# Kernel tuning notes

Measured on AMD Instinct MI355X. Metric: run time of the kernel, lower is better.

The kernel has to match this reference:

```python
import jax, jax.numpy as jnp
import numpy as np

EPS = 1e-5


def setup_inputs() -> dict:
    key = jax.random.key(0)
    ks = jax.random.split(key, 8)
    B, C, D, H, O, E = 256, 64, 256, 4096, 256, 4
    x = jax.random.normal(ks[0], (B, C, D), dtype=jnp.float32)
    mask_ids = jax.random.randint(ks[1], (B, C), 0, 16)
    projection_idx = jax.random.randint(ks[2], (C,), 0, E)
    W1 = jax.random.normal(ks[3], (E, D, H), dtype=jnp.float32) * 0.02
    b1 = jnp.zeros((E, H), dtype=jnp.float32)
    gamma = jnp.ones((E, H), dtype=jnp.float32)
    beta = jnp.zeros((E, H), dtype=jnp.float32)
    W2 = jax.random.normal(ks[4], (E, H, O), dtype=jnp.float32) * 0.02
    b2 = jnp.zeros((E, O), dtype=jnp.float32)
    return {"x": x, "mask_ids": mask_ids, "projection_idx": projection_idx,
            "W1": W1, "b1": b1, "gamma": gamma, "beta": beta, "W2": W2, "b2": b2}


def reference(x, mask_ids, projection_idx, W1, b1, gamma, beta, W2, b2):
    # x: [B, C, D]; projection_idx: [C] routes each channel to one of E experts.
    # Disjoint masks => the original zeros + masked '+=' is a partition-assign.
    B, C, D = x.shape
    E, _, H = W1.shape
    # Per-channel expert params (gather once, shared over batch).
    h = jnp.einsum('bcd,cdh->bch', x, W1[projection_idx]) + b1[projection_idx]
    # BatchNorm1d in training mode: batch stats over the tokens of each expert
    # (the original flattens the selected [B, |mask|] tokens for BN).
    seg = jnp.broadcast_to(projection_idx[None, :], (B, C)).reshape(-1)  # [B*C]
    hf = h.reshape(B * C, H)
    cnt = jax.ops.segment_sum(jnp.ones((B * C,), h.dtype), seg, num_segments=E)
    cnt = jnp.maximum(cnt, 1.0)
    s1 = jax.ops.segment_sum(hf, seg, num_segments=E)            # [E, H]
    s2 = jax.ops.segment_sum(hf * hf, seg, num_segments=E)       # [E, H]
    mean = s1 / cnt[:, None]
    var = s2 / cnt[:, None] - mean * mean                        # biased var (train-mode BN)
    inv = jax.lax.rsqrt(var + EPS)
    hn = (h - mean[projection_idx]) * (inv[projection_idx] * gamma[projection_idx]) + beta[projection_idx]
    a = jax.nn.relu(hn)
    out = jnp.einsum('bch,cho->bco', a, W2[projection_idx]) + b2[projection_idx]
    return out, mask_ids
```

## Files before the change

kernel.cpp:

```cpp
#include <hip/hip_runtime.h>

typedef unsigned short u16;
typedef unsigned int   u32;
typedef __attribute__((ext_vector_type(8))) short s16x8;
typedef __attribute__((ext_vector_type(4))) float f32x4;
typedef __attribute__((ext_vector_type(4))) u32   u32x4;

#define DEV static __device__ __forceinline__

static constexpr int B_ = 256, C_ = 64, D_ = 256, H_ = 4096, O_ = 256, E_ = 4;

DEV u16 f2bf(float f) {
  u32 u = __builtin_bit_cast(u32, f);
  u += 0x7fffu + ((u >> 16) & 1u);
  return (u16)(u >> 16);
}
DEV float bf2f(u16 u) { return __builtin_bit_cast(float, (u32)u << 16); }

DEV void async16(const u16* g, u16* l) {
  __builtin_amdgcn_global_load_lds(
      (const __attribute__((address_space(1))) void*)g,
      (__attribute__((address_space(3))) void*)l, 16, 0, 0);
}

DEV int xcd_swz(int bid, int nwg) { return (bid & 7) * (nwg >> 3) + (bid >> 3); }

__global__ void k_prep(const float* __restrict__ x, u16* __restrict__ xb,
                       const float* __restrict__ W1, u16* __restrict__ w1t,
                       const float* __restrict__ W2, u16* __restrict__ w2t,
                       const int* __restrict__ proj, int* __restrict__ perm) {
  __shared__ float tile[64][65];
  const int bx = blockIdx.x, tid = threadIdx.x;
  if (bx < 2048) {
    const int i = bx * 256 + tid;
    const f32x4 a = ((const f32x4*)x)[2 * i];
    const f32x4 b = ((const f32x4*)x)[2 * i + 1];
    u32x4 o;
    o[0] = (u32)f2bf(a[0]) | ((u32)f2bf(a[1]) << 16);
    o[1] = (u32)f2bf(a[2]) | ((u32)f2bf(a[3]) << 16);
    o[2] = (u32)f2bf(b[0]) | ((u32)f2bf(b[1]) << 16);
    o[3] = (u32)f2bf(b[2]) | ((u32)f2bf(b[3]) << 16);
    ((u32x4*)xb)[i] = o;
    return;
  }
  if (bx < 4096) {
    const bool w1 = bx < 3072;
    const int R  = w1 ? D_ : H_;
    const int Cc = w1 ? H_ : O_;
    const float* s0 = w1 ? W1 : W2;
    u16* d0 = w1 ? w1t : w2t;
    int b = bx - (w1 ? 2048 : 3072);
    const int nct = Cc >> 6, nrt = R >> 6;
    const int ct = b % nct; b /= nct;
    const int rt = b % nrt; const int e = b / nrt;
    const float* s = s0 + (size_t)e * R * Cc;
    u16* d = d0 + (size_t)e * R * Cc;
    const int tx = tid & 63, ty = tid >> 6;
    #pragma unroll
    for (int i = 0; i < 64; i += 4)
      tile[i + ty][tx] = s[(size_t)(rt * 64 + i + ty) * Cc + ct * 64 + tx];
    __syncthreads();
    #pragma unroll
    for (int i = 0; i < 64; i += 4) {
      const int cc = i + ty;
      d[(size_t)(ct * 64 + cc) * R + rt * 64 + tx] = f2bf(tile[tx][cc]);
    }
    return;
  }
  if (tid < C_) {
    const int e = proj[tid];
    int rank = 0;
    for (int c2 = 0; c2 < C_; ++c2) {
      const int e2 = proj[c2];
      rank += (e2 < e) || (e2 == e && c2 < tid);
    }
    perm[rank] = tid;
  }
}

__global__ __launch_bounds__(256, 4)
void k_gemm1(const u16* __restrict__ A, const u16* __restrict__ Bw,
             const int* __restrict__ proj, const int* __restrict__ perm,
             const float* __restrict__ bias,
             u16* __restrict__ outH, float* __restrict__ s1p, float* __restrict__ s2p) {
  constexpr int BM = 128, BN = 128, BK = 32, KT = D_ / BK;
  constexpr int SA = BM * BK / 8, SB = BN * BK / 8;
  constexpr int BUF = (SA + SB) * 8;
  __shared__ __align__(16) u16 lds[2 * BUF];
  __shared__ float stash[2][4][16][2];
  const int tid = threadIdx.x, l = tid & 63, w = tid >> 6, wm = w >> 1, wn = w & 1;

  int bid = xcd_swz(blockIdx.x, gridDim.x);
  constexpr int NT = H_ / BN, BT = B_ / BM;
  const int nt = bid % NT; bid /= NT;
  const int bt = bid % BT; const int ci = bid / BT;
  const int c = perm[ci];
  const int e = proj[c];

  const size_t rsA = (size_t)C_ * D_;
  const u16* Ab = A + (size_t)c * D_ + (size_t)bt * BM * rsA;
  const u16* Bb = Bw + ((size_t)e * H_ + (size_t)nt * BN) * D_;

  f32x4 acc[4][4] = {};

  auto stage = [&](int kt) {
    const int k0 = kt * BK;
    u16* dst = lds + (kt & 1) * BUF;
    #pragma unroll
    for (int i = 0; i < 2; ++i) {
      const int s = i * 256 + tid, row = s >> 2, j = (s & 3) ^ ((row >> 1) & 3);
      async16(Ab + (size_t)row * rsA + k0 + j * 8, dst + s * 8);
    }
    #pragma unroll
    for (int i = 0; i < 2; ++i) {
      const int s = i * 256 + tid, col = s >> 2, j = (s & 3) ^ ((col >> 1) & 3);
      async16(Bb + (size_t)col * D_ + k0 + j * 8, dst + SA * 8 + s * 8);
    }
  };

  stage(0);
  asm volatile("s_waitcnt vmcnt(0)" ::: "memory");
  __builtin_amdgcn_s_barrier();

  #pragma unroll
  for (int kt = 0; kt < KT; ++kt) {
    if (kt + 1 < KT) stage(kt + 1);
    const u16* bufA = lds + (kt & 1) * BUF;
    const u16* bufB = bufA + SA * 8;
    s16x8 av[4], bv[4];
    #pragma unroll
    for (int m = 0; m < 4; ++m) {
      const int r = wm * 64 + m * 16 + (l & 15), p = (l >> 4) ^ ((r >> 1) & 3);
      av[m] = *(const s16x8*)(bufA + (r * 4 + p) * 8);
    }
    #pragma unroll
    for (int n = 0; n < 4; ++n) {
      const int cc = wn * 64 + n * 16 + (l & 15), p = (l >> 4) ^ ((cc >> 1) & 3);
      bv[n] = *(const s16x8*)(bufB + (cc * 4 + p) * 8);
    }
    #pragma unroll
    for (int m = 0; m < 4; ++m)
      #pragma unroll
      for (int n = 0; n < 4; ++n)
        acc[m][n] = __builtin_amdgcn_mfma_f32_16x16x32_bf16(av[m], bv[n], acc[m][n], 0, 0, 0);
    asm volatile("s_waitcnt vmcnt(0) lgkmcnt(0)" ::: "memory");
    __builtin_amdgcn_s_barrier();
  }

  u16* ldsOut = lds;
  float p1s[4], p2s[4];
  #pragma unroll
  for (int n = 0; n < 4; ++n) {
    const int colL = wn * 64 + n * 16 + (l & 15);
    const int colg = nt * BN + colL;
    const float bval = bias[e * H_ + colg];
    float p1 = 0.f, p2 = 0.f;
    #pragma unroll
    for (int m = 0; m < 4; ++m) {
      const int rbase = wm * 64 + m * 16 + (l >> 4) * 4;
      #pragma unroll
      for (int i = 0; i < 4; ++i) {
        const float v = acc[m][n][i] + bval;
        p1 += v; p2 += v * v;
        const int row = rbase + i;
        const int phys = (colL >> 3) ^ (row & 15);
        ldsOut[row * 128 + phys * 8 + (colL & 7)] = f2bf(v);
      }
    }
    p1 += __shfl_xor(p1, 16); p1 += __shfl_xor(p1, 32);
    p2 += __shfl_xor(p2, 16); p2 += __shfl_xor(p2, 32);
    if (wm == 1 && l < 16) { stash[wn][n][l & 15][0] = p1; stash[wn][n][l & 15][1] = p2; }
    p1s[n] = p1; p2s[n] = p2;
  }
  __syncthreads();
  if (wm == 0 && l < 16) {
    const int rowp = c * 2 + bt;
    #pragma unroll
    for (int n = 0; n < 4; ++n) {
      const int colg = nt * BN + wn * 64 + n * 16 + (l & 15);
      s1p[(size_t)rowp * H_ + colg] = p1s[n] + stash[wn][n][l & 15][0];
      s2p[(size_t)rowp * H_ + colg] = p2s[n] + stash[wn][n][l & 15][1];
    }
  }
  u16* outB = outH + ((size_t)c * B_ + (size_t)bt * BM) * H_ + nt * BN;
  #pragma unroll
  for (int pass = 0; pass < 8; ++pass) {
    const int row = pass * 16 + (tid >> 4), sl = tid & 15;
    const u32x4 v = *(const u32x4*)(ldsOut + row * 128 + ((sl ^ (row & 15)) * 8));
    *(u32x4*)(outB + (size_t)row * H_ + sl * 8) = v;
  }
}

__global__ void k_finalize(const float* __restrict__ s1p, const float* __restrict__ s2p,
                           const int* __restrict__ proj, const float* __restrict__ gamma,
                           const float* __restrict__ beta,
                           u16* __restrict__ sclB, u16* __restrict__ shfB) {
  const int i = blockIdx.x * 256 + threadIdx.x;
  const int e = i >> 12;
  const int hcol = i & 4095;
  int cn = 0;
  float q1 = 0.f, q2 = 0.f;
  for (int c = 0; c < C_; ++c) {
    if (proj[c] == e) {
      ++cn;
      q1 += s1p[(size_t)(c * 2) * H_ + hcol] + s1p[(size_t)(c * 2 + 1) * H_ + hcol];
      q2 += s2p[(size_t)(c * 2) * H_ + hcol] + s2p[(size_t)(c * 2 + 1) * H_ + hcol];
    }
  }
  const float cnt = fmaxf((float)cn * (float)B_, 1.f);
  const float mean = q1 / cnt;
  const float var = q2 / cnt - mean * mean;
  const float sc = rsqrtf(var + 1e-5f) * gamma[i];
  sclB[i] = f2bf(sc);
  shfB[i] = f2bf(beta[i] - mean * sc);
}

template<int KS>
__global__ __launch_bounds__(256, 4)
void k_gemm2(const u16* __restrict__ A, const u16* __restrict__ Bw,
             const int* __restrict__ proj, const int* __restrict__ perm,
             const float* __restrict__ b2,
             const u16* __restrict__ scB, const u16* __restrict__ shB,
             float* __restrict__ outF, float* __restrict__ partial) {
  constexpr int BM = 128, BN = 128, BK = 32, KH = H_ / KS, KT = KH / BK;
  constexpr int SA = BM * BK / 8, SB = BN * BK / 8;
  constexpr int BUF = (SA + SB) * 8;
  __shared__ __align__(16) u16 lds[2 * BUF + 2 * KH];
  u16* stS = lds + 2 * BUF;
  u16* stT = stS + KH;
  const int tid = threadIdx.x, l = tid & 63, w = tid >> 6, wm = w >> 1, wn = w & 1;

  int bid = xcd_swz(blockIdx.x, gridDim.x);
  const int ks = bid & (KS - 1); bid /= KS;
  const int nt = bid & 1; bid >>= 1;
  const int bt = bid & 1; const int ci = bid >> 1;
  const int c = perm[ci];
  const int e = proj[c];

  const size_t rsA = (size_t)H_;
  const u16* Ab = A + ((size_t)c * B_ + (size_t)bt * BM) * H_ + (size_t)ks * KH;
  const u16* Bb = Bw + ((size_t)e * O_ + (size_t)nt * BN) * H_ + (size_t)ks * KH;
  const u16* scE = scB + e * H_ + ks * KH;
  const u16* shE = shB + e * H_ + ks * KH;

  f32x4 acc[4][4] = {};
  s16x8 h0[2], h1[2], b0r[2], b1r[2];

  auto Aissue = [&](int kt, s16x8 (&hs)[2]) {
    const int k0 = kt * BK;
    #pragma unroll
    for (int i = 0; i < 2; ++i) {
      const int s = i * 256 + tid, row = s >> 2, j = (s & 3) ^ ((row >> 1) & 3);
      hs[i] = *(const s16x8*)(Ab + (size_t)row * rsA + k0 + j * 8);
    }
  };
  auto Bissue = [&](int kt, s16x8 (&bs)[2]) {
    const int k0 = kt * BK;
    #pragma unroll
    for (int i = 0; i < 2; ++i) {
      const int s = i * 256 + tid, col = s >> 2, j = (s & 3) ^ ((col >> 1) & 3);
      bs[i] = *(const s16x8*)(Bb + (size_t)col * H_ + k0 + j * 8);
    }
  };
  auto Awrite = [&](int kt, s16x8 (&hs)[2]) {
    u16* dst = lds + (kt & 1) * BUF;
    const int k0 = kt * BK;
    #pragma unroll
    for (int i = 0; i < 2; ++i) {
      const int s = i * 256 + tid, row = s >> 2, j = (s & 3) ^ ((row >> 1) & 3);
      const s16x8 sv = *(const s16x8*)(stS + k0 + j * 8);
      const s16x8 tv = *(const s16x8*)(stT + k0 + j * 8);
      u32x4 o;
      #pragma unroll
      for (int jj = 0; jj < 4; ++jj) {
        const float v0 = fmaxf(bf2f((u16)hs[i][2 * jj]) * bf2f((u16)sv[2 * jj]) + bf2f((u16)tv[2 * jj]), 0.f);
        const float v1 = fmaxf(bf2f((u16)hs[i][2 * jj + 1]) * bf2f((u16)sv[2 * jj + 1]) + bf2f((u16)tv[2 * jj + 1]), 0.f);
        o[jj] = (u32)f2bf(v0) | ((u32)f2bf(v1) << 16);
      }
      *(u32x4*)(dst + s * 8) = o;
    }
  };
  auto Bwrite = [&](int kt, s16x8 (&bs)[2]) {
    u16* dst = lds + (kt & 1) * BUF + SA * 8;
    #pragma unroll
    for (int i = 0; i < 2; ++i) {
      const int s = i * 256 + tid;
      *(u32x4*)(dst + s * 8) = __builtin_bit_cast(u32x4, bs[i]);
    }
  };
  auto Compute = [&](int kt) {
    const u16* bufA = lds + (kt & 1) * BUF;
    const u16* bufB = bufA + SA * 8;
    s16x8 av[4], bv[4];
    #pragma unroll
    for (int m = 0; m < 4; ++m) {
      const int r = wm * 64 + m * 16 + (l & 15), p = (l >> 4) ^ ((r >> 1) & 3);
      av[m] = *(const s16x8*)(bufA + (r * 4 + p) * 8);
    }
    #pragma unroll
    for (int n = 0; n < 4; ++n) {
      const int cc = wn * 64 + n * 16 + (l & 15), p = (l >> 4) ^ ((cc >> 1) & 3);
      bv[n] = *(const s16x8*)(bufB + (cc * 4 + p) * 8);
    }
    #pragma unroll
    for (int m = 0; m < 4; ++m)
      #pragma unroll
      for (int n = 0; n < 4; ++n)
        acc[m][n] = __builtin_amdgcn_mfma_f32_16x16x32_bf16(av[m], bv[n], acc[m][n], 0, 0, 0);
  };

  for (int q = tid; q < KH / 4; q += 256) {
    if (q < KH / 8) async16(scE + q * 8, stS + q * 8);
    else            async16(shE + (q - KH / 8) * 8, stT + (q - KH / 8) * 8);
  }
  Aissue(0, h0); Bissue(0, b0r);
  Aissue(1, h1); Bissue(1, b1r);
  asm volatile("s_waitcnt vmcnt(0)" ::: "memory");
  __builtin_amdgcn_s_barrier();
  Awrite(0, h0); Bwrite(0, b0r);
  asm volatile("s_waitcnt lgkmcnt(0)" ::: "memory");
  __builtin_amdgcn_s_barrier();

  #pragma unroll 1
  for (int kt = 0; kt + 3 < KT; kt += 2) {
    Aissue(kt + 2, h0); Bissue(kt + 2, b0r);
    Compute(kt);
    Awrite(kt + 1, h1); Bwrite(kt + 1, b1r);
    asm volatile("s_waitcnt lgkmcnt(0)" ::: "memory");
    __builtin_amdgcn_s_barrier();
    Aissue(kt + 3, h1); Bissue(kt + 3, b1r);
    Compute(kt + 1);
    Awrite(kt + 2, h0); Bwrite(kt + 2, b0r);
    asm volatile("s_waitcnt lgkmcnt(0)" ::: "memory");
    __builtin_amdgcn_s_barrier();
  }

  Compute(KT - 2);
  Awrite(KT - 1, h1); Bwrite(KT - 1, b1r);
  asm volatile("s_waitcnt lgkmcnt(0)" ::: "memory");
  __builtin_amdgcn_s_barrier();
  Compute(KT - 1);

  float* dstF = ks ? (partial + (size_t)(ks - 1) * B_ * C_ * O_) : outF;
  #pragma unroll
  for (int n = 0; n < 4; ++n) {
    const int colg = nt * BN + wn * 64 + n * 16 + (l & 15);
    const float bval = ks ? 0.f : b2[e * O_ + colg];
    #pragma unroll
    for (int m = 0; m < 4; ++m) {
      #pragma unroll
      for (int i = 0; i < 4; ++i) {
        const int rg = bt * BM + wm * 64 + m * 16 + (l >> 4) * 4 + i;
        dstF[((size_t)rg * C_ + c) * O_ + colg] = acc[m][n][i] + bval;
      }
    }
  }
}

__global__ void k_combine(float* __restrict__ out, const float* __restrict__ partial,
                          const int nparts, const int* __restrict__ mask,
                          float* __restrict__ maskOut) {
  const int gi = blockIdx.x * 256 + threadIdx.x;
  const size_t b = (size_t)gi * 2;
  constexpr size_t PARTV = (size_t)B_ * C_ * O_ / 4;
  f32x4 a0 = ((const f32x4*)out)[b], a1 = ((const f32x4*)out)[b + 1];
  for (int p = 0; p < nparts; ++p) {
    const f32x4 p0 = ((const f32x4*)partial)[p * PARTV + b];
    const f32x4 p1 = ((const f32x4*)partial)[p * PARTV + b + 1];
    #pragma unroll
    for (int j = 0; j < 4; ++j) { a0[j] += p0[j]; a1[j] += p1[j]; }
  }
  ((f32x4*)out)[b] = a0; ((f32x4*)out)[b + 1] = a1;
  if (gi < B_ * C_ / 8) {
    #pragma unroll
    for (int j = 0; j < 8; ++j) maskOut[gi * 8 + j] = (float)mask[gi * 8 + j];
  }
}

extern "C" void kernel_launch(void* const* d_in, const int* in_sizes, int n_in,
                              void* d_out, int out_size, void* d_ws, size_t ws_size,
                              hipStream_t stream) {
  const float* x     = (const float*)d_in[0];
  const int*   mask  = (const int*)d_in[1];
  const int*   proj  = (const int*)d_in[2];
  const float* W1    = (const float*)d_in[3];
  const float* b1    = (const float*)d_in[4];
  const float* gamma = (const float*)d_in[5];
  const float* beta  = (const float*)d_in[6];
  const float* W2    = (const float*)d_in[7];
  const float* b2    = (const float*)d_in[8];
  float* out = (float*)d_out;

  char* ws = (char*)d_ws;
  size_t off = 0;
  u16* hbuf = (u16*)(ws + off); off += (size_t)B_ * C_ * H_ * 2;
  u16* xb   = (u16*)(ws + off); off += (size_t)B_ * C_ * D_ * 2;
  u16* w1t  = (u16*)(ws + off); off += (size_t)E_ * D_ * H_ * 2;
  float* partial2 = (float*)xb;
  u16* w2t  = (u16*)(ws + off); off += (size_t)E_ * H_ * O_ * 2;
  float* s1p = (float*)(ws + off); off += (size_t)2 * C_ * H_ * 4;
  float* s2p = (float*)(ws + off); off += (size_t)2 * C_ * H_ * 4;
  u16* sclB = (u16*)(ws + off); off += (size_t)E_ * H_ * 2;
  u16* shfB = (u16*)(ws + off); off += (size_t)E_ * H_ * 2;
  int* perm = (int*)(ws + off); off += 256;
  off = (off + 255) & ~(size_t)255;
  float* partial4 = (float*)(ws + off);
  const bool ks4 = ws_size >= off + (size_t)3 * B_ * C_ * O_ * 4;


  k_prep<<<4097, 256, 0, stream>>>(x, xb, W1, w1t, W2, w2t, proj, perm);

  k_gemm1<<<C_ * 2 * 32, 256, 0, stream>>>(xb, w1t, proj, perm, b1, hbuf, s1p, s2p);

  k_finalize<<<E_ * H_ / 256, 256, 0, stream>>>(s1p, s2p, proj, gamma, beta, sclB, shfB);

  if (ks4) {
    k_gemm2<4><<<1024, 256, 0, stream>>>(hbuf, w2t, proj, perm, b2, sclB, shfB, out, partial4);
    k_combine<<<B_ * C_ * O_ / 8 / 256, 256, 0, stream>>>(out, partial4, 3, mask,
                                                          out + (size_t)B_ * C_ * O_);
  } else {
    k_gemm2<2><<<512, 256, 0, stream>>>(hbuf, w2t, proj, perm, b2, sclB, shfB, out, partial2);
    k_combine<<<B_ * C_ * O_ / 8 / 256, 256, 0, stream>>>(out, partial2, 1, mask,
                                                          out + (size_t)B_ * C_ * O_);
  }
}
```

Baseline: 177.8 us.

## Reshape GEMM2 tiles to 64x256 so each A row is normalized once

Changes the second GEMM tile from 128x128 to 64x256, so each block covers the full output width and the BN+ReLU transform on A is applied once per row rather than twice across two N-tiles. It also removes the 4-way split-K path and always uses the 2-way split, which shrinks the partial buffer and the combine pass. Launch bounds drop to 2 blocks per CU to make room for the larger B staging. The costs are more B-tile loads per block and lower occupancy, and with the fixed 2-way split some parallelism is lost when a larger workspace is available.

```diff
diff --git a/kernel.cpp b/kernel.cpp
--- a/kernel.cpp
+++ b/kernel.cpp
@@ -216,74 +216,66 @@
 }
 
 template<int KS>
-__global__ __launch_bounds__(256, 4)
+__global__ __launch_bounds__(256, 2)
 void k_gemm2(const u16* __restrict__ A, const u16* __restrict__ Bw,
              const int* __restrict__ proj, const int* __restrict__ perm,
              const float* __restrict__ b2,
              const u16* __restrict__ scB, const u16* __restrict__ shB,
              float* __restrict__ outF, float* __restrict__ partial) {
-  constexpr int BM = 128, BN = 128, BK = 32, KH = H_ / KS, KT = KH / BK;
+  constexpr int BM = 64, BN = 256, BK = 32, KH = H_ / KS, KT = KH / BK;
   constexpr int SA = BM * BK / 8, SB = BN * BK / 8;
   constexpr int BUF = (SA + SB) * 8;
   __shared__ __align__(16) u16 lds[2 * BUF + 2 * KH];
   u16* stS = lds + 2 * BUF;
   u16* stT = stS + KH;
-  const int tid = threadIdx.x, l = tid & 63, w = tid >> 6, wm = w >> 1, wn = w & 1;
+  const int tid = threadIdx.x, l = tid & 63, w = tid >> 6;
 
   int bid = xcd_swz(blockIdx.x, gridDim.x);
   const int ks = bid & (KS - 1); bid /= KS;
-  const int nt = bid & 1; bid >>= 1;
-  const int bt = bid & 1; const int ci = bid >> 1;
+  const int bt = bid & 3; const int ci = bid >> 2;
   const int c = perm[ci];
   const int e = proj[c];
 
-  const size_t rsA = (size_t)H_;
   const u16* Ab = A + ((size_t)c * B_ + (size_t)bt * BM) * H_ + (size_t)ks * KH;
-  const u16* Bb = Bw + ((size_t)e * O_ + (size_t)nt * BN) * H_ + (size_t)ks * KH;
+  const u16* Bb = Bw + (size_t)e * O_ * H_ + (size_t)ks * KH;
   const u16* scE = scB + e * H_ + ks * KH;
   const u16* shE = shB + e * H_ + ks * KH;
 
   f32x4 acc[4][4] = {};
-  s16x8 h0[2], h1[2], b0r[2], b1r[2];
-
-  auto Aissue = [&](int kt, s16x8 (&hs)[2]) {
+  s16x8 h0[1], h1[1], b0r[4], b1r[4];
+
+  auto Aissue = [&](int kt, s16x8 (&hs)[1]) {
     const int k0 = kt * BK;
-    #pragma unroll
-    for (int i = 0; i < 2; ++i) {
-      const int s = i * 256 + tid, row = s >> 2, j = (s & 3) ^ ((row >> 1) & 3);
-      hs[i] = *(const s16x8*)(Ab + (size_t)row * rsA + k0 + j * 8);
-    }
-  };
-  auto Bissue = [&](int kt, s16x8 (&bs)[2]) {
+    const int s = tid, row = s >> 2, j = (s & 3) ^ ((row >> 1) & 3);
+    hs[0] = *(const s16x8*)(Ab + (size_t)row * H_ + k0 + j * 8);
+  };
+  auto Bissue = [&](int kt, s16x8 (&bs)[4]) {
     const int k0 = kt * BK;
     #pragma unroll
-    for (int i = 0; i < 2; ++i) {
+    for (int i = 0; i < 4; ++i) {
       const int s = i * 256 + tid, col = s >> 2, j = (s & 3) ^ ((col >> 1) & 3);
       bs[i] = *(const s16x8*)(Bb + (size_t)col * H_ + k0 + j * 8);
     }
   };
-  auto Awrite = [&](int kt, s16x8 (&hs)[2]) {
+  auto Awrite = [&](int kt, s16x8 (&hs)[1]) {
     u16* dst = lds + (kt & 1) * BUF;
     const int k0 = kt * BK;
-    #pragma unroll
-    for (int i = 0; i < 2; ++i) {
-      const int s = i * 256 + tid, row = s >> 2, j = (s & 3) ^ ((row >> 1) & 3);
-      const s16x8 sv = *(const s16x8*)(stS + k0 + j * 8);
-      const s16x8 tv = *(const s16x8*)(stT + k0 + j * 8);
-      u32x4 o;
-      #pragma unroll
-      for (int jj = 0; jj < 4; ++jj) {
-        const float v0 = fmaxf(bf2f((u16)hs[i][2 * jj]) * bf2f((u16)sv[2 * jj]) + bf2f((u16)tv[2 * jj]), 0.f);
-        const float v1 = fmaxf(bf2f((u16)hs[i][2 * jj + 1]) * bf2f((u16)sv[2 * jj + 1]) + bf2f((u16)tv[2 * jj + 1]), 0.f);
-        o[jj] = (u32)f2bf(v0) | ((u32)f2bf(v1) << 16);
-      }
-      *(u32x4*)(dst + s * 8) = o;
-    }
-  };
-  auto Bwrite = [&](int kt, s16x8 (&bs)[2]) {
+    const int s = tid, j = (s & 3) ^ (((s >> 2) >> 1) & 3);
+    const s16x8 sv = *(const s16x8*)(stS + k0 + j * 8);
+    const s16x8 tv = *(const s16x8*)(stT + k0 + j * 8);
+    u32x4 o;
+    #pragma unroll
+    for (int jj = 0; jj < 4; ++jj) {
+      const float v0 = fmaxf(bf2f((u16)hs[0][2 * jj]) * bf2f((u16)sv[2 * jj]) + bf2f((u16)tv[2 * jj]), 0.f);
+      const float v1 = fmaxf(bf2f((u16)hs[0][2 * jj + 1]) * bf2f((u16)sv[2 * jj + 1]) + bf2f((u16)tv[2 * jj + 1]), 0.f);
+      o[jj] = (u32)f2bf(v0) | ((u32)f2bf(v1) << 16);
+    }
+    *(u32x4*)(dst + s * 8) = o;
+  };
+  auto Bwrite = [&](int kt, s16x8 (&bs)[4]) {
     u16* dst = lds + (kt & 1) * BUF + SA * 8;
     #pragma unroll
-    for (int i = 0; i < 2; ++i) {
+    for (int i = 0; i < 4; ++i) {
       const int s = i * 256 + tid;
       *(u32x4*)(dst + s * 8) = __builtin_bit_cast(u32x4, bs[i]);
     }
@@ -294,12 +286,12 @@
     s16x8 av[4], bv[4];
     #pragma unroll
     for (int m = 0; m < 4; ++m) {
-      const int r = wm * 64 + m * 16 + (l & 15), p = (l >> 4) ^ ((r >> 1) & 3);
+      const int r = m * 16 + (l & 15), p = (l >> 4) ^ ((r >> 1) & 3);
       av[m] = *(const s16x8*)(bufA + (r * 4 + p) * 8);
     }
     #pragma unroll
     for (int n = 0; n < 4; ++n) {
-      const int cc = wn * 64 + n * 16 + (l & 15), p = (l >> 4) ^ ((cc >> 1) & 3);
+      const int cc = w * 64 + n * 16 + (l & 15), p = (l >> 4) ^ ((cc >> 1) & 3);
       bv[n] = *(const s16x8*)(bufB + (cc * 4 + p) * 8);
     }
     #pragma unroll
@@ -341,16 +333,16 @@
   __builtin_amdgcn_s_barrier();
   Compute(KT - 1);
 
-  float* dstF = ks ? (partial + (size_t)(ks - 1) * B_ * C_ * O_) : outF;
+  float* dstF = ks ? partial : outF;
   #pragma unroll
   for (int n = 0; n < 4; ++n) {
-    const int colg = nt * BN + wn * 64 + n * 16 + (l & 15);
+    const int colg = w * 64 + n * 16 + (l & 15);
     const float bval = ks ? 0.f : b2[e * O_ + colg];
     #pragma unroll
     for (int m = 0; m < 4; ++m) {
       #pragma unroll
       for (int i = 0; i < 4; ++i) {
-        const int rg = bt * BM + wm * 64 + m * 16 + (l >> 4) * 4 + i;
+        const int rg = bt * BM + m * 16 + (l >> 4) * 4 + i;
         dstF[((size_t)rg * C_ + c) * O_ + colg] = acc[m][n][i] + bval;
       }
     }
@@ -358,18 +350,13 @@
 }
 
 __global__ void k_combine(float* __restrict__ out, const float* __restrict__ partial,
-                          const int nparts, const int* __restrict__ mask,
-                          float* __restrict__ maskOut) {
+                          const int* __restrict__ mask, float* __restrict__ maskOut) {
   const int gi = blockIdx.x * 256 + threadIdx.x;
   const size_t b = (size_t)gi * 2;
-  constexpr size_t PARTV = (size_t)B_ * C_ * O_ / 4;
   f32x4 a0 = ((const f32x4*)out)[b], a1 = ((const f32x4*)out)[b + 1];
-  for (int p = 0; p < nparts; ++p) {
-    const f32x4 p0 = ((const f32x4*)partial)[p * PARTV + b];
-    const f32x4 p1 = ((const f32x4*)partial)[p * PARTV + b + 1];
-    #pragma unroll
-    for (int j = 0; j < 4; ++j) { a0[j] += p0[j]; a1[j] += p1[j]; }
-  }
+  const f32x4 p0 = ((const f32x4*)partial)[b], p1 = ((const f32x4*)partial)[b + 1];
+  #pragma unroll
+  for (int j = 0; j < 4; ++j) { a0[j] += p0[j]; a1[j] += p1[j]; }
   ((f32x4*)out)[b] = a0; ((f32x4*)out)[b + 1] = a1;
   if (gi < B_ * C_ / 8) {
     #pragma unroll
@@ -396,16 +383,13 @@
   u16* hbuf = (u16*)(ws + off); off += (size_t)B_ * C_ * H_ * 2;
   u16* xb   = (u16*)(ws + off); off += (size_t)B_ * C_ * D_ * 2;
   u16* w1t  = (u16*)(ws + off); off += (size_t)E_ * D_ * H_ * 2;
-  float* partial2 = (float*)xb;
+  float* partial = (float*)xb;
   u16* w2t  = (u16*)(ws + off); off += (size_t)E_ * H_ * O_ * 2;
   float* s1p = (float*)(ws + off); off += (size_t)2 * C_ * H_ * 4;
   float* s2p = (float*)(ws + off); off += (size_t)2 * C_ * H_ * 4;
   u16* sclB = (u16*)(ws + off); off += (size_t)E_ * H_ * 2;
   u16* shfB = (u16*)(ws + off); off += (size_t)E_ * H_ * 2;
   int* perm = (int*)(ws + off); off += 256;
-  off = (off + 255) & ~(size_t)255;
-  float* partial4 = (float*)(ws + off);
-  const bool ks4 = ws_size >= off + (size_t)3 * B_ * C_ * O_ * 4;
 
 
   k_prep<<<4097, 256, 0, stream>>>(x, xb, W1, w1t, W2, w2t, proj, perm);
@@ -414,13 +398,8 @@
 
   k_finalize<<<E_ * H_ / 256, 256, 0, stream>>>(s1p, s2p, proj, gamma, beta, sclB, shfB);
 
-  if (ks4) {
-    k_gemm2<4><<<1024, 256, 0, stream>>>(hbuf, w2t, proj, perm, b2, sclB, shfB, out, partial4);
-    k_combine<<<B_ * C_ * O_ / 8 / 256, 256, 0, stream>>>(out, partial4, 3, mask,
-                                                          out + (size_t)B_ * C_ * O_);
-  } else {
-    k_gemm2<2><<<512, 256, 0, stream>>>(hbuf, w2t, proj, perm, b2, sclB, shfB, out, partial2);
-    k_combine<<<B_ * C_ * O_ / 8 / 256, 256, 0, stream>>>(out, partial2, 1, mask,
-                                                          out + (size_t)B_ * C_ * O_);
-  }
-}
+  k_gemm2<2><<<512, 256, 0, stream>>>(hbuf, w2t, proj, perm, b2, sclB, shfB, out, partial);
+
+  k_combine<<<B_ * C_ * O_ / 8 / 256, 256, 0, stream>>>(out, partial, mask,
+                                                        out + (size_t)B_ * C_ * O_);
+}
```

After: 158.4 us. -10.9%, faster.
